# Kernel tuning notes

Measured on AMD Instinct MI355X. Metric: run time of the kernel, lower is better.

## Reference

```python
import jax, jax.numpy as jnp
import numpy as np

DIM = 512
H = 8
D = 64
EPS = 1e-5


def _ln(x, g, b):
    m = jnp.mean(x, axis=-1, keepdims=True)
    v = jnp.var(x, axis=-1, keepdims=True)
    return (x - m) * jax.lax.rsqrt(v + EPS) * g + b


def _attn(x, ctx, wq, wk, wv, wo, bo):
    B, S, _ = x.shape
    T = ctx.shape[1]
    q = (x @ wq).reshape(B, S, H, D)
    k = (ctx @ wk).reshape(B, T, H, D)
    v = (ctx @ wv).reshape(B, T, H, D)
    scale = D ** -0.5
    score = jnp.einsum('bqhd,bkhd->bhqk', q, k) * scale  # [B,H,S,T]
    w = jax.nn.softmax(score, axis=-1)
    o = jnp.einsum('bhqk,bkhd->bqhd', w, v).reshape(B, S, H * D)
    return o @ wo + bo


def _geglu(x, w, b):
    h = x @ w + b
    y, gate = h[..., :4 * DIM], h[..., 4 * DIM:]
    tanh_res = jnp.tanh(gate * 0.7978845608 * (1.0 + 0.044715 * gate * gate))
    return y * 0.5 * gate * (1.0 + tanh_res)


def setup_inputs() -> dict:
    key = jax.random.key(0)
    ks = jax.random.split(key, 16)
    s = 0.02
    inp = {
        'x': jax.random.normal(ks[0], (2, 4096, DIM), jnp.float32),
        'context': jax.random.normal(ks[1], (2, 77, DIM), jnp.float32),
        'ln1_g': jnp.ones((DIM,), jnp.float32),
        'ln1_b': jnp.zeros((DIM,), jnp.float32),
        'wq1': jax.random.normal(ks[2], (DIM, H * D), jnp.float32) * s,
        'wk1': jax.random.normal(ks[3], (DIM, H * D), jnp.float32) * s,
        'wv1': jax.random.normal(ks[4], (DIM, H * D), jnp.float32) * s,
        'wo1': jax.random.normal(ks[5], (H * D, H * D), jnp.float32) * s,
        'bo1': jnp.zeros((H * D,), jnp.float32),
        'ln2_g': jnp.ones((DIM,), jnp.float32),
        'ln2_b': jnp.zeros((DIM,), jnp.float32),
        'wq2': jax.random.normal(ks[6], (DIM, H * D), jnp.float32) * s,
        'wk2': jax.random.normal(ks[7], (DIM, H * D), jnp.float32) * s,
        'wv2': jax.random.normal(ks[8], (DIM, H * D), jnp.float32) * s,
        'wo2': jax.random.normal(ks[9], (H * D, H * D), jnp.float32) * s,
        'bo2': jnp.zeros((H * D,), jnp.float32),
        'ln3_g': jnp.ones((DIM,), jnp.float32),
        'ln3_b': jnp.zeros((DIM,), jnp.float32),
        'geglu_w': jax.random.normal(ks[10], (DIM, 8 * DIM), jnp.float32) * s,
        'geglu_b': jnp.zeros((8 * DIM,), jnp.float32),
        'out_w': jax.random.normal(ks[11], (4 * DIM, DIM), jnp.float32) * s,
        'out_b': jnp.zeros((DIM,), jnp.float32),
    }
    return inp


def reference(x, context, ln1_g, ln1_b, wq1, wk1, wv1, wo1, bo1,
              ln2_g, ln2_b, wq2, wk2, wv2, wo2, bo2,
              ln3_g, ln3_b, geglu_w, geglu_b, out_w, out_b):
    h = _attn(_ln(x, ln1_g, ln1_b), _ln(x, ln1_g, ln1_b), wq1, wk1, wv1, wo1, bo1) + x
    h = _attn(_ln(h, ln2_g, ln2_b), context, wq2, wk2, wv2, wo2, bo2) + h
    ff = _geglu(_ln(h, ln3_g, ln3_b), geglu_w, geglu_b)
    return ff @ out_w + out_b + h
```

## Files before the change

### kernel.cpp

```cpp
#include <hip/hip_runtime.h>
#include <hip/hip_bf16.h>
#include <math.h>

#define DIM 512
#define NHEAD 8
#define HD 64
#define BATCH 2
#define SEQ 4096
#define CTXLEN 77
#define NTOK (BATCH*SEQ)
#define NCTX (BATCH*CTXLEN)

typedef __hip_bfloat16 bf16;
typedef __attribute__((ext_vector_type(8))) short bf8_t;
typedef __attribute__((ext_vector_type(4))) float f4_t;

__device__ __forceinline__ float b2f(bf16 v){ return __bfloat162float(v); }
__device__ __forceinline__ bf16  f2b(float v){ return __float2bfloat16(v); }
__device__ __forceinline__ unsigned int packbf2(float a, float b){
    unsigned int au = __float_as_uint(a) + 0x8000u;
    unsigned int bu = __float_as_uint(b) + 0x8000u;
    return __builtin_amdgcn_perm(bu, au, 0x07060302u);
}
__device__ __forceinline__ void  stf(float* p, float v){ *p = v; }
__device__ __forceinline__ void  stf(bf16* p, float v){ *p = f2b(v); }

__device__ __forceinline__ void glds16(const bf16* g, unsigned short* l){
    __builtin_amdgcn_global_load_lds(
        (__attribute__((address_space(1))) void*)g,
        (__attribute__((address_space(3))) void*)l,
        16, 0, 0);
}

__global__ __launch_bounds__(256)
void ln_kernel(const float* __restrict__ x, const float* __restrict__ g,
               const float* __restrict__ b, bf16* __restrict__ out, int nrows)
{
    int row  = blockIdx.x * 4 + (threadIdx.x >> 6);
    int lane = threadIdx.x & 63;
    if (row >= nrows) return;
    const float* xr = x + (size_t)row * DIM;
    float v[8];
    float s = 0.f, sq = 0.f;
    #pragma unroll
    for (int j = 0; j < 8; ++j) {
        float f = xr[lane + 64*j];
        v[j] = f; s += f; sq += f*f;
    }
    #pragma unroll
    for (int off = 32; off; off >>= 1) {
        s  += __shfl_xor(s,  off);
        sq += __shfl_xor(sq, off);
    }
    float mean = s * (1.f/DIM);
    float var  = sq * (1.f/DIM) - mean*mean;
    float rstd = rsqrtf(var + 1e-5f);
    bf16* orow = out + (size_t)row * DIM;
    #pragma unroll
    for (int j = 0; j < 8; ++j) {
        int c = lane + 64*j;
        orow[c] = f2b((v[j]-mean)*rstd*g[c] + b[c]);
    }
}

__global__ __launch_bounds__(256)
void transpose_bf16_kernel(const float* __restrict__ W, bf16* __restrict__ Wt, int K, int N)
{
    __shared__ float tile[32][33];
    int n0 = blockIdx.x * 32, k0 = blockIdx.y * 32;
    int tx = threadIdx.x & 31, ty = threadIdx.x >> 5;
    #pragma unroll
    for (int p = 0; p < 4; ++p)
        tile[ty + p*8][tx] = W[(size_t)(k0 + ty + p*8)*N + n0 + tx];
    __syncthreads();
    #pragma unroll
    for (int p = 0; p < 4; ++p)
        Wt[(size_t)(n0 + ty + p*8)*K + k0 + tx] = f2b(tile[tx][ty + p*8]);
}

struct TPtrs { const float* src[8]; bf16* dst[8]; };
__global__ __launch_bounds__(256)
void transpose8_kernel(TPtrs p)
{
    __shared__ float tile[32][33];
    const float* W = p.src[blockIdx.z];
    bf16* Wt = p.dst[blockIdx.z];
    int n0 = blockIdx.x * 32, k0 = blockIdx.y * 32;
    int tx = threadIdx.x & 31, ty = threadIdx.x >> 5;
    #pragma unroll
    for (int q = 0; q < 4; ++q)
        tile[ty + q*8][tx] = W[(size_t)(k0 + ty + q*8)*512 + n0 + tx];
    __syncthreads();
    #pragma unroll
    for (int q = 0; q < 4; ++q)
        Wt[(size_t)(n0 + ty + q*8)*512 + k0 + tx] = f2b(tile[tx][ty + q*8]);
}

__global__ __launch_bounds__(256)
void cast_bf16_kernel(const float* __restrict__ in, bf16* __restrict__ out, int n)
{
    int i = blockIdx.x*256 + threadIdx.x;
    if (i < n) out[i] = f2b(in[i]);
}

__global__ __launch_bounds__(256)
void v_transpose_kernel(const bf16* __restrict__ V, bf16* __restrict__ Vt, int T, int pitch)
{
    __shared__ __align__(16) unsigned short tile[64*64];
    const int tid = threadIdx.x;
    const int b = blockIdx.z, h = blockIdx.y;
    const int t0 = blockIdx.x * 64;
    #pragma unroll
    for (int it = 0; it < 2; ++it) {
        int e = tid + it*256;
        int t = e >> 3, c = e & 7;
        int gk = t0 + t;
        bf8_t v = {0,0,0,0,0,0,0,0};
        if (gk < T) v = *(const bf8_t*)(V + ((size_t)(b*T + gk))*DIM + h*HD + c*8);
        *(bf8_t*)&tile[t*64 + c*8] = v;
    }
    __syncthreads();
    #pragma unroll
    for (int it = 0; it < 2; ++it) {
        int e = tid + it*256;
        int d = e & 63, oc = e >> 6;
        unsigned short tmp[8];
        #pragma unroll
        for (int j = 0; j < 8; ++j) tmp[j] = tile[(oc*8 + j)*64 + d];
        *(bf8_t*)(Vt + ((size_t)((b*8 + h)*64 + d))*pitch + t0 + oc*8) = *(bf8_t*)tmp;
    }
}

struct OutPtrs { void* p[3]; };
template<int RESID, typename OUTT, bool GUARD>
__global__ __launch_bounds__(256)
void gemm_mfma_kernel(const bf16* __restrict__ A, const bf16* __restrict__ Wt,
                      const float* __restrict__ bias, const float* __restrict__ resid,
                      OutPtrs outs, int M, int K)
{
    __shared__ __align__(16) unsigned short As[2][128*64];
    __shared__ __align__(16) unsigned short Bs[2][64*64];
    const int tid  = threadIdx.x;
    const int wave = tid >> 6, lane = tid & 63;
    const int l16  = lane & 15, quad = lane >> 4;
    const int wm = (wave >> 1) * 64, wn = (wave & 1) * 32;
    const int m0 = blockIdx.y * 128, n0 = blockIdx.x * 64;
    OUTT* outp = (OUTT*)outs.p[n0 >> 9];
    const int lc0 = n0 & 511;
    const int lr = lane >> 3;
    const int lc = (lane & 7) ^ lr;

    f4_t acc[4][2];
    #pragma unroll
    for (int i = 0; i < 4; ++i) { acc[i][0] = f4_t{0,0,0,0}; acc[i][1] = f4_t{0,0,0,0}; }

    auto stage = [&](int k0, int bf) {
        #pragma unroll
        for (int i = 0; i < 4; ++i) {
            int r = (wave*4 + i)*8 + lr;
            int gr = m0 + r;
            if (GUARD) gr = (gr < M) ? gr : (M-1);
            glds16(A + (size_t)gr*K + k0 + lc*8, &As[bf][(wave*4 + i)*512]);
        }
        #pragma unroll
        for (int j = 0; j < 2; ++j) {
            int r = (wave*2 + j)*8 + lr;
            glds16(Wt + (size_t)(n0 + r)*K + k0 + lc*8, &Bs[bf][(wave*2 + j)*512]);
        }
    };

    stage(0, 0);
    __syncthreads();

    for (int k0 = 0; k0 < K; k0 += 64) {
        const int bf = (k0 >> 6) & 1;
        if (k0 + 64 < K) stage(k0 + 64, bf ^ 1);
        #pragma unroll
        for (int kc = 0; kc < 2; ++kc) {
            const int cg = kc*4 + quad;
            bf8_t af[4], bfr[2];
            #pragma unroll
            for (int mt = 0; mt < 4; ++mt) {
                int r = wm + mt*16 + l16;
                af[mt] = *(const bf8_t*)&As[bf][r*64 + ((cg ^ (r&7))*8)];
            }
            #pragma unroll
            for (int nt = 0; nt < 2; ++nt) {
                int r = wn + nt*16 + l16;
                bfr[nt] = *(const bf8_t*)&Bs[bf][r*64 + ((cg ^ (r&7))*8)];
            }
            #pragma unroll
            for (int mt = 0; mt < 4; ++mt)
                #pragma unroll
                for (int nt = 0; nt < 2; ++nt)
                    acc[mt][nt] = __builtin_amdgcn_mfma_f32_16x16x32_bf16(af[mt], bfr[nt], acc[mt][nt], 0, 0, 0);
        }
        __syncthreads();
    }

    #pragma unroll
    for (int mt = 0; mt < 4; ++mt) {
        #pragma unroll
        for (int r_ = 0; r_ < 4; ++r_) {
            int row = m0 + wm + mt*16 + quad*4 + r_;
            if (GUARD && row >= M) continue;
            size_t rb = (size_t)row * 512;
            #pragma unroll
            for (int nt = 0; nt < 2; ++nt) {
                int col = lc0 + wn + nt*16 + l16;
                float v = acc[mt][nt][r_];
                if (bias) v += bias[col];
                if (RESID) v += resid[rb + col];
                stf(&outp[rb + col], v);
            }
        }
    }
}

__global__ __launch_bounds__(256)
void geglu_mfma_kernel(const bf16* __restrict__ A, const bf16* __restrict__ WtG,
                       const float* __restrict__ bias, bf16* __restrict__ outp)
{
    __shared__ __align__(16) unsigned short As[128*64];
    __shared__ __align__(16) unsigned short Bys[64*64];
    __shared__ __align__(16) unsigned short Bgs[64*64];
    const int tid  = threadIdx.x;
    const int wave = tid >> 6, lane = tid & 63;
    const int l16  = lane & 15, quad = lane >> 4;
    const int m0 = blockIdx.y * 128, n0 = blockIdx.x * 64;
    const int lr = lane >> 3;
    const int lc = (lane & 7) ^ lr;

    f4_t accy[2][4], accg[2][4];
    #pragma unroll
    for (int i = 0; i < 2; ++i)
        #pragma unroll
        for (int j = 0; j < 4; ++j) { accy[i][j] = f4_t{0,0,0,0}; accg[i][j] = f4_t{0,0,0,0}; }

    for (int k0 = 0; k0 < DIM; k0 += 64) {
        #pragma unroll
        for (int i = 0; i < 4; ++i) {
            int r = (wave*4 + i)*8 + lr;
            glds16(A + (size_t)(m0 + r)*DIM + k0 + lc*8, &As[(wave*4 + i)*512]);
        }
        #pragma unroll
        for (int j = 0; j < 2; ++j) {
            int r = (wave*2 + j)*8 + lr;
            glds16(WtG + (size_t)(n0 + r)*DIM + k0 + lc*8, &Bys[(wave*2 + j)*512]);
            glds16(WtG + (size_t)(2048 + n0 + r)*DIM + k0 + lc*8, &Bgs[(wave*2 + j)*512]);
        }
        __syncthreads();
        #pragma unroll
        for (int kc = 0; kc < 2; ++kc) {
            const int cg = kc*4 + quad;
            bf8_t af[2];
            #pragma unroll
            for (int mt = 0; mt < 2; ++mt) {
                int r = wave*32 + mt*16 + l16;
                af[mt] = *(const bf8_t*)&As[r*64 + ((cg ^ (r&7))*8)];
            }
            #pragma unroll
            for (int nt = 0; nt < 4; ++nt) {
                int r = nt*16 + l16;
                bf8_t by = *(const bf8_t*)&Bys[r*64 + ((cg ^ (r&7))*8)];
                bf8_t bg = *(const bf8_t*)&Bgs[r*64 + ((cg ^ (r&7))*8)];
                #pragma unroll
                for (int mt = 0; mt < 2; ++mt) {
                    accy[mt][nt] = __builtin_amdgcn_mfma_f32_16x16x32_bf16(af[mt], by, accy[mt][nt], 0, 0, 0);
                    accg[mt][nt] = __builtin_amdgcn_mfma_f32_16x16x32_bf16(af[mt], bg, accg[mt][nt], 0, 0, 0);
                }
            }
        }
        __syncthreads();
    }

    #pragma unroll
    for (int mt = 0; mt < 2; ++mt) {
        #pragma unroll
        for (int r_ = 0; r_ < 4; ++r_) {
            int row = m0 + wave*32 + mt*16 + quad*4 + r_;
            size_t rb = (size_t)row * 2048;
            #pragma unroll
            for (int nt = 0; nt < 4; ++nt) {
                int col = n0 + nt*16 + l16;
                float y = accy[mt][nt][r_] + bias[col];
                float g = accg[mt][nt][r_] + bias[2048 + col];
                float t = tanhf(0.7978845608f*g*(1.f + 0.044715f*g*g));
                outp[rb + col] = f2b(y * 0.5f * g * (1.f + t));
            }
        }
    }
}

__global__ __launch_bounds__(512)
void attn_mfma_kernel(const bf16* __restrict__ Qm, const bf16* __restrict__ Km,
                      const bf16* __restrict__ VtG, bf16* __restrict__ Om,
                      int T, int vpitch)
{
    __shared__ __align__(16) unsigned short Ks[2][64*64];
    __shared__ __align__(16) unsigned short Vts[2][64*64];

    const int tid  = threadIdx.x;
    const int wave = tid >> 6, lane = tid & 63;
    const int l16  = lane & 15, quad = lane >> 4;
    const int b = blockIdx.z, h = blockIdx.y;
    const int qblk = blockIdx.x * 128;
    const int lr = lane >> 3;
    const int lc = (lane & 7) ^ lr;
    const int srow = wave*8 + lr;

    bf8_t ones;
    #pragma unroll
    for (int j = 0; j < 8; ++j) ((unsigned short*)&ones)[j] = 0x3F80;

    bf8_t qf[2];
    {
        const bf16* qp = Qm + ((size_t)(b*SEQ + qblk + wave*16 + l16))*DIM + h*HD + quad*8;
        #pragma unroll
        for (int kc = 0; kc < 2; ++kc) {
            bf8_t v = *(const bf8_t*)(qp + kc*32);
            unsigned short* u = (unsigned short*)&v;
            unsigned int* w = (unsigned int*)&v;
            #pragma unroll
            for (int j = 0; j < 4; ++j) {
                float f0 = b2f(*(bf16*)&u[2*j])   * 0.1803368801f;
                float f1 = b2f(*(bf16*)&u[2*j+1]) * 0.1803368801f;
                w[j] = packbf2(f0, f1);
            }
            qf[kc] = v;
        }
    }

    f4_t o[4];
    #pragma unroll
    for (int dt = 0; dt < 4; ++dt) o[dt] = f4_t{0,0,0,0};
    f4_t lacc = {0,0,0,0};

    const bf16* Kbase = Km + (size_t)b*T*DIM + h*HD;
    const bf16* Vbase = VtG + ((size_t)((b*8 + h)*64 + srow))*vpitch;

    {
        int gk = srow; if (gk > T-1) gk = T-1;
        glds16(Kbase + (size_t)gk*DIM + lc*8, &Ks[0][wave*512]);
        glds16(Vbase + lc*8,                  &Vts[0][wave*512]);
    }
    __syncthreads();

    const int ntiles = (T + 63) >> 6;
    for (int t0 = 0; t0 < ntiles; ++t0) {
        const int kb = t0 << 6;
        const int cur = t0 & 1;
        if (t0 + 1 < ntiles) {
            int gk = kb + 64 + srow; if (gk > T-1) gk = T-1;
            glds16(Kbase + (size_t)gk*DIM + lc*8,  &Ks[cur^1][wave*512]);
            glds16(Vbase + kb + 64 + lc*8,         &Vts[cur^1][wave*512]);
        }

        bf8_t kf[4][2], vf[4][2];
        #pragma unroll
        for (int t = 0; t < 4; ++t) {
            int r = t*16 + l16;
            #pragma unroll
            for (int kc = 0; kc < 2; ++kc) {
                int cg = kc*4 + quad;
                kf[t][kc] = *(const bf8_t*)&Ks[cur][r*64 + ((cg ^ (r&7))*8)];
                vf[t][kc] = *(const bf8_t*)&Vts[cur][r*64 + ((cg ^ (r&7))*8)];
            }
        }
        const bool tail = (kb + 64 > T);

        f4_t sc4[4];
        #pragma unroll
        for (int km = 0; km < 4; ++km) {
            f4_t c = {0,0,0,0};
            c = __builtin_amdgcn_mfma_f32_16x16x32_bf16(kf[km][0], qf[0], c, 0, 0, 0);
            c = __builtin_amdgcn_mfma_f32_16x16x32_bf16(kf[km][1], qf[1], c, 0, 0, 0);
            sc4[km] = c;
        }
        if (tail) {
            #pragma unroll
            for (int km = 0; km < 4; ++km)
                #pragma unroll
                for (int r = 0; r < 4; ++r)
                    if (kb + km*16 + quad*4 + r >= T) sc4[km][r] = -1e30f;
        }
        unsigned int pk[4][2];
        #pragma unroll
        for (int km = 0; km < 4; ++km) {
            pk[km][0] = packbf2(exp2f(sc4[km][0]), exp2f(sc4[km][1]));
            pk[km][1] = packbf2(exp2f(sc4[km][2]), exp2f(sc4[km][3]));
        }
        #pragma unroll
        for (int kc = 0; kc < 2; ++kc) {
            auto s0 = __builtin_amdgcn_permlane32_swap(pk[2*kc][0], pk[2*kc+1][0], false, false);
            auto w02 = __builtin_amdgcn_permlane16_swap(s0[0], s0[1], false, false);
            auto s1 = __builtin_amdgcn_permlane32_swap(pk[2*kc][1], pk[2*kc+1][1], false, false);
            auto w13 = __builtin_amdgcn_permlane16_swap(s1[0], s1[1], false, false);
            union { unsigned int u[4]; bf8_t v; } pfu;
            pfu.u[0] = w02[0]; pfu.u[1] = w13[0]; pfu.u[2] = w02[1]; pfu.u[3] = w13[1];
            bf8_t pf = pfu.v;
            lacc = __builtin_amdgcn_mfma_f32_16x16x32_bf16(ones, pf, lacc, 0, 0, 0);
            #pragma unroll
            for (int dt = 0; dt < 4; ++dt)
                o[dt] = __builtin_amdgcn_mfma_f32_16x16x32_bf16(vf[dt][kc], pf, o[dt], 0, 0, 0);
        }
        __syncthreads();
    }

    {
        float inv = 1.f / lacc[0];
        int tok = qblk + wave*16 + l16;
        size_t base = ((size_t)(b*SEQ + tok))*DIM + h*HD;
        #pragma unroll
        for (int dt = 0; dt < 4; ++dt) {
            uint2 w;
            w.x = packbf2(o[dt][0]*inv, o[dt][1]*inv);
            w.y = packbf2(o[dt][2]*inv, o[dt][3]*inv);
            *(uint2*)(Om + base + dt*16 + quad*4) = w;
        }
    }
}

extern "C" void kernel_launch(void* const* d_in, const int* in_sizes, int n_in,
                              void* d_out, int out_size, void* d_ws, size_t ws_size,
                              hipStream_t stream)
{
    (void)in_sizes; (void)n_in; (void)out_size; (void)ws_size;
    const float* x    = (const float*)d_in[0];
    const float* ctx  = (const float*)d_in[1];
    const float* ln1g = (const float*)d_in[2];
    const float* ln1b = (const float*)d_in[3];
    const float* wq1  = (const float*)d_in[4];
    const float* wk1  = (const float*)d_in[5];
    const float* wv1  = (const float*)d_in[6];
    const float* wo1  = (const float*)d_in[7];
    const float* bo1  = (const float*)d_in[8];
    const float* ln2g = (const float*)d_in[9];
    const float* ln2b = (const float*)d_in[10];
    const float* wq2  = (const float*)d_in[11];
    const float* wk2  = (const float*)d_in[12];
    const float* wv2  = (const float*)d_in[13];
    const float* wo2  = (const float*)d_in[14];
    const float* bo2  = (const float*)d_in[15];
    const float* ln3g = (const float*)d_in[16];
    const float* ln3b = (const float*)d_in[17];
    const float* gw   = (const float*)d_in[18];
    const float* gb   = (const float*)d_in[19];
    const float* ow   = (const float*)d_in[20];
    const float* ob   = (const float*)d_in[21];
    float* out = (float*)d_out;

    char* ws = (char*)d_ws;
    bf16* An  = (bf16*)(ws);
    bf16* VtG = (bf16*)(ws);
    bf16* Qb  = (bf16*)(ws + ((size_t)8<<20));
    bf16* Kb  = (bf16*)(ws + ((size_t)16<<20));
    bf16* Vb  = (bf16*)(ws + ((size_t)24<<20));
    bf16* Ob  = (bf16*)(ws + ((size_t)32<<20));
    bf16* FF  = Qb;
    float* Hf = out;
    bf16* WT  = (bf16*)(ws + ((size_t)40<<20));
    bf16* wq1T = WT + 0*262144, *wk1T = WT + 1*262144, *wv1T = WT + 2*262144, *wo1T = WT + 3*262144;
    bf16* wq2T = WT + 4*262144, *wk2T = WT + 5*262144, *wv2T = WT + 6*262144, *wo2T = WT + 7*262144;
    bf16* gwT  = (bf16*)(ws + ((size_t)44<<20));
    bf16* owT  = (bf16*)(ws + ((size_t)48<<20));
    bf16* ctxb = (bf16*)(ws + ((size_t)50<<20));
    bf16* VtG2 = (bf16*)(ws + ((size_t)50<<20) + ((size_t)512<<10));

    dim3 blk(256);
    dim3 blkA(512);

    TPtrs tp;
    tp.src[0]=wq1; tp.src[1]=wk1; tp.src[2]=wv1; tp.src[3]=wo1;
    tp.src[4]=wq2; tp.src[5]=wk2; tp.src[6]=wv2; tp.src[7]=wo2;
    tp.dst[0]=wq1T; tp.dst[1]=wk1T; tp.dst[2]=wv1T; tp.dst[3]=wo1T;
    tp.dst[4]=wq2T; tp.dst[5]=wk2T; tp.dst[6]=wv2T; tp.dst[7]=wo2T;
    transpose8_kernel<<<dim3(16,16,8), blk, 0, stream>>>(tp);
    transpose_bf16_kernel<<<dim3(128,16), blk, 0, stream>>>(gw, gwT, DIM, 4096);
    transpose_bf16_kernel<<<dim3(16,64), blk, 0, stream>>>(ow, owT, 2048, DIM);
    cast_bf16_kernel<<<dim3((NCTX*DIM+255)/256), blk, 0, stream>>>(ctx, ctxb, NCTX*DIM);

    dim3 gLN(NTOK/4);
    dim3 gQKV(24, 64);
    dim3 gG(8, 64);
    dim3 gKVx(16, 2);
    dim3 gGEGLU(32, 64);
    dim3 gATT(SEQ/128, NHEAD, BATCH);
    OutPtrs oQKV{{Qb, Kb, Vb}};
    OutPtrs oKVx{{Kb, Vb, nullptr}};
    OutPtrs oQ{{Qb, nullptr, nullptr}};
    OutPtrs oH{{Hf, nullptr, nullptr}};
    OutPtrs oOut{{out, nullptr, nullptr}};

    ln_kernel<<<gLN, blk, 0, stream>>>(x, ln1g, ln1b, An, NTOK);
    gemm_mfma_kernel<0,bf16,false><<<gQKV, blk, 0, stream>>>(An, wq1T, nullptr, nullptr, oQKV, NTOK, DIM);
    v_transpose_kernel<<<dim3(SEQ/64, NHEAD, BATCH), blk, 0, stream>>>(Vb, VtG, SEQ, SEQ);
    attn_mfma_kernel<<<gATT, blkA, 0, stream>>>(Qb, Kb, VtG, Ob, SEQ, SEQ);
    gemm_mfma_kernel<1,float,false><<<gG, blk, 0, stream>>>(Ob, wo1T, bo1, x, oH, NTOK, DIM);

    ln_kernel<<<gLN, blk, 0, stream>>>(Hf, ln2g, ln2b, An, NTOK);
    gemm_mfma_kernel<0,bf16,false><<<gG, blk, 0, stream>>>(An, wq2T, nullptr, nullptr, oQ, NTOK, DIM);
    gemm_mfma_kernel<0,bf16,true><<<gKVx, blk, 0, stream>>>(ctxb, wk2T, nullptr, nullptr, oKVx, NCTX, DIM);
    v_transpose_kernel<<<dim3(2, NHEAD, BATCH), blk, 0, stream>>>(Vb, VtG2, CTXLEN, 128);
    attn_mfma_kernel<<<gATT, blkA, 0, stream>>>(Qb, Kb, VtG2, Ob, CTXLEN, 128);
    gemm_mfma_kernel<1,float,false><<<gG, blk, 0, stream>>>(Ob, wo2T, bo2, Hf, oH, NTOK, DIM);

    ln_kernel<<<gLN, blk, 0, stream>>>(Hf, ln3g, ln3b, An, NTOK);
    geglu_mfma_kernel<<<gGEGLU, blk, 0, stream>>>(An, gwT, gb, FF);
    gemm_mfma_kernel<1,float,false><<<gG, blk, 0, stream>>>(FF, owT, ob, Hf, oOut, NTOK, 2048);
}
```

Measured before the change: 472.2 us.

## Split self-attention over two key halves with a combine pass, restructure K/V staging

The self-attention kernel now splits the key range into two halves across extra blocks, writes unnormalized fp32 partial outputs and row sums, and a new combine kernel sums and normalizes them. The aim is more blocks and more parallelism for the long-sequence attention. K/V staging switches from double-buffered async global-to-LDS loads to register prefetch into a single LDS buffer. The P-matrix transpose moves from permlane swaps to an LDS round-trip. The price is extra fp32 partial-output traffic, one more launch, and an extra sync plus LDS writes per tile.

```diff
diff --git a/kernel.cpp b/kernel.cpp
--- a/kernel.cpp
+++ b/kernel.cpp
@@ -292,22 +292,26 @@
     }
 }
 
-__global__ __launch_bounds__(512)
+template<bool SPLITW>
+__global__ __launch_bounds__(512, 8)
 void attn_mfma_kernel(const bf16* __restrict__ Qm, const bf16* __restrict__ Km,
                       const bf16* __restrict__ VtG, bf16* __restrict__ Om,
+                      float* __restrict__ OP, float* __restrict__ LP,
                       int T, int vpitch)
 {
-    __shared__ __align__(16) unsigned short Ks[2][64*64];
-    __shared__ __align__(16) unsigned short Vts[2][64*64];
+    __shared__ __align__(16) unsigned short Ks[64*64];
+    __shared__ __align__(16) unsigned short Vts[64*64];
+    __shared__ __align__(16) unsigned short Ps[8][16*64];
 
     const int tid  = threadIdx.x;
     const int wave = tid >> 6, lane = tid & 63;
     const int l16  = lane & 15, quad = lane >> 4;
-    const int b = blockIdx.z, h = blockIdx.y;
+    int b, s, TT, t_lo;
+    if (SPLITW) { s = blockIdx.z >> 1; b = blockIdx.z & 1; TT = T >> 1; t_lo = s * TT; }
+    else        { s = 0; b = blockIdx.z; TT = T; t_lo = 0; }
+    const int h = blockIdx.y;
     const int qblk = blockIdx.x * 128;
-    const int lr = lane >> 3;
-    const int lc = (lane & 7) ^ lr;
-    const int srow = wave*8 + lr;
+    const int sr = tid >> 3, sc_ = tid & 7;
 
     bf8_t ones;
     #pragma unroll
@@ -336,24 +340,25 @@
     for (int dt = 0; dt < 4; ++dt) o[dt] = f4_t{0,0,0,0};
     f4_t lacc = {0,0,0,0};
 
-    const bf16* Kbase = Km + (size_t)b*T*DIM + h*HD;
-    const bf16* Vbase = VtG + ((size_t)((b*8 + h)*64 + srow))*vpitch;
-
-    {
-        int gk = srow; if (gk > T-1) gk = T-1;
-        glds16(Kbase + (size_t)gk*DIM + lc*8, &Ks[0][wave*512]);
-        glds16(Vbase + lc*8,                  &Vts[0][wave*512]);
-    }
-    __syncthreads();
-
-    const int ntiles = (T + 63) >> 6;
+    const bf16* Kbase = Km + ((size_t)b*T + t_lo)*DIM + h*HD;
+    const bf16* Vbase = VtG + ((size_t)((b*8 + h)*64 + sr))*vpitch + t_lo;
+
+    bf8_t kq, vq;
+    kq = bf8_t{0,0,0,0,0,0,0,0};
+    if (sr < TT) kq = *(const bf8_t*)(Kbase + (size_t)sr*DIM + sc_*8);
+    vq = *(const bf8_t*)(Vbase + sc_*8);
+
+    const int ntiles = (TT + 63) >> 6;
     for (int t0 = 0; t0 < ntiles; ++t0) {
         const int kb = t0 << 6;
-        const int cur = t0 & 1;
+        *(bf8_t*)&Ks[sr*64 + ((sc_ ^ (sr&7))*8)]  = kq;
+        *(bf8_t*)&Vts[sr*64 + ((sc_ ^ (sr&7))*8)] = vq;
+        __syncthreads();
         if (t0 + 1 < ntiles) {
-            int gk = kb + 64 + srow; if (gk > T-1) gk = T-1;
-            glds16(Kbase + (size_t)gk*DIM + lc*8,  &Ks[cur^1][wave*512]);
-            glds16(Vbase + kb + 64 + lc*8,         &Vts[cur^1][wave*512]);
+            int gk = kb + 64 + sr;
+            kq = bf8_t{0,0,0,0,0,0,0,0};
+            if (gk < TT) kq = *(const bf8_t*)(Kbase + (size_t)gk*DIM + sc_*8);
+            vq = *(const bf8_t*)(Vbase + kb + 64 + sc_*8);
         }
 
         bf8_t kf[4][2], vf[4][2];
@@ -363,11 +368,11 @@
             #pragma unroll
             for (int kc = 0; kc < 2; ++kc) {
                 int cg = kc*4 + quad;
-                kf[t][kc] = *(const bf8_t*)&Ks[cur][r*64 + ((cg ^ (r&7))*8)];
-                vf[t][kc] = *(const bf8_t*)&Vts[cur][r*64 + ((cg ^ (r&7))*8)];
-            }
-        }
-        const bool tail = (kb + 64 > T);
+                kf[t][kc] = *(const bf8_t*)&Ks[r*64 + ((cg ^ (r&7))*8)];
+                vf[t][kc] = *(const bf8_t*)&Vts[r*64 + ((cg ^ (r&7))*8)];
+            }
+        }
+        const bool tail = (kb + 64 > TT);
 
         f4_t sc4[4];
         #pragma unroll
@@ -382,23 +387,21 @@
             for (int km = 0; km < 4; ++km)
                 #pragma unroll
                 for (int r = 0; r < 4; ++r)
-                    if (kb + km*16 + quad*4 + r >= T) sc4[km][r] = -1e30f;
-        }
-        unsigned int pk[4][2];
+                    if (kb + km*16 + quad*4 + r >= TT) sc4[km][r] = -1e30f;
+        }
         #pragma unroll
         for (int km = 0; km < 4; ++km) {
-            pk[km][0] = packbf2(exp2f(sc4[km][0]), exp2f(sc4[km][1]));
-            pk[km][1] = packbf2(exp2f(sc4[km][2]), exp2f(sc4[km][3]));
+            uint2 w;
+            w.x = packbf2(exp2f(sc4[km][0]), exp2f(sc4[km][1]));
+            w.y = packbf2(exp2f(sc4[km][2]), exp2f(sc4[km][3]));
+            int chunk = 2*km + (quad >> 1);
+            int a = l16*64 + ((chunk ^ (l16 & 7))*8) + (quad & 1)*4;
+            *(uint2*)&Ps[wave][a] = w;
         }
         #pragma unroll
         for (int kc = 0; kc < 2; ++kc) {
-            auto s0 = __builtin_amdgcn_permlane32_swap(pk[2*kc][0], pk[2*kc+1][0], false, false);
-            auto w02 = __builtin_amdgcn_permlane16_swap(s0[0], s0[1], false, false);
-            auto s1 = __builtin_amdgcn_permlane32_swap(pk[2*kc][1], pk[2*kc+1][1], false, false);
-            auto w13 = __builtin_amdgcn_permlane16_swap(s1[0], s1[1], false, false);
-            union { unsigned int u[4]; bf8_t v; } pfu;
-            pfu.u[0] = w02[0]; pfu.u[1] = w13[0]; pfu.u[2] = w02[1]; pfu.u[3] = w13[1];
-            bf8_t pf = pfu.v;
+            int cg = kc*4 + quad;
+            bf8_t pf = *(const bf8_t*)&Ps[wave][l16*64 + ((cg ^ (l16 & 7))*8)];
             lacc = __builtin_amdgcn_mfma_f32_16x16x32_bf16(ones, pf, lacc, 0, 0, 0);
             #pragma unroll
             for (int dt = 0; dt < 4; ++dt)
@@ -407,9 +410,16 @@
         __syncthreads();
     }
 
-    {
+    const int tok = qblk + wave*16 + l16;
+    if (SPLITW) {
+        size_t obase = ((size_t)((s*BATCH + b)*SEQ) + tok)*DIM + h*HD;
+        #pragma unroll
+        for (int dt = 0; dt < 4; ++dt)
+            *(f4_t*)(OP + obase + dt*16 + quad*4) = o[dt];
+        if (quad == 0)
+            LP[((size_t)((s*BATCH + b)*SEQ) + tok)*NHEAD + h] = lacc[0];
+    } else {
         float inv = 1.f / lacc[0];
-        int tok = qblk + wave*16 + l16;
         size_t base = ((size_t)(b*SEQ + tok))*DIM + h*HD;
         #pragma unroll
         for (int dt = 0; dt < 4; ++dt) {
@@ -419,6 +429,26 @@
             *(uint2*)(Om + base + dt*16 + quad*4) = w;
         }
     }
+}
+
+__global__ __launch_bounds__(256)
+void attn_combine_kernel(const float* __restrict__ OP, const float* __restrict__ LP,
+                         bf16* __restrict__ Om)
+{
+    const size_t NP = (size_t)BATCH*SEQ*DIM;
+    int i = blockIdx.x*256 + threadIdx.x;
+    size_t e = (size_t)i * 4;
+    int bt = (int)(e >> 9);
+    int d  = (int)(e & 511);
+    int hh = d >> 6;
+    f4_t a0 = *(const f4_t*)(OP + (size_t)bt*DIM + d);
+    f4_t a1 = *(const f4_t*)(OP + NP + (size_t)bt*DIM + d);
+    float l = LP[(size_t)bt*NHEAD + hh] + LP[(size_t)BATCH*SEQ*NHEAD + (size_t)bt*NHEAD + hh];
+    float inv = 1.f / l;
+    uint2 w;
+    w.x = packbf2((a0[0]+a1[0])*inv, (a0[1]+a1[1])*inv);
+    w.y = packbf2((a0[2]+a1[2])*inv, (a0[3]+a1[3])*inv);
+    *(uint2*)(Om + e) = w;
 }
 
 extern "C" void kernel_launch(void* const* d_in, const int* in_sizes, int n_in,
@@ -466,6 +496,8 @@
     bf16* owT  = (bf16*)(ws + ((size_t)48<<20));
     bf16* ctxb = (bf16*)(ws + ((size_t)50<<20));
     bf16* VtG2 = (bf16*)(ws + ((size_t)50<<20) + ((size_t)512<<10));
+    float* OP  = (float*)(ws + ((size_t)52<<20));
+    float* LP  = (float*)(ws + ((size_t)86<<20));
 
     dim3 blk(256);
     dim3 blkA(512);
@@ -486,6 +518,8 @@
     dim3 gKVx(16, 2);
     dim3 gGEGLU(32, 64);
     dim3 gATT(SEQ/128, NHEAD, BATCH);
+    dim3 gATTs(SEQ/128, NHEAD, BATCH*2);
+    dim3 gCMB(NTOK*DIM/4/256);
     OutPtrs oQKV{{Qb, Kb, Vb}};
     OutPtrs oKVx{{Kb, Vb, nullptr}};
     OutPtrs oQ{{Qb, nullptr, nullptr}};
@@ -495,14 +529,15 @@
     ln_kernel<<<gLN, blk, 0, stream>>>(x, ln1g, ln1b, An, NTOK);
     gemm_mfma_kernel<0,bf16,false><<<gQKV, blk, 0, stream>>>(An, wq1T, nullptr, nullptr, oQKV, NTOK, DIM);
     v_transpose_kernel<<<dim3(SEQ/64, NHEAD, BATCH), blk, 0, stream>>>(Vb, VtG, SEQ, SEQ);
-    attn_mfma_kernel<<<gATT, blkA, 0, stream>>>(Qb, Kb, VtG, Ob, SEQ, SEQ);
+    attn_mfma_kernel<true><<<gATTs, blkA, 0, stream>>>(Qb, Kb, VtG, Ob, OP, LP, SEQ, SEQ);
+    attn_combine_kernel<<<gCMB, blk, 0, stream>>>(OP, LP, Ob);
     gemm_mfma_kernel<1,float,false><<<gG, blk, 0, stream>>>(Ob, wo1T, bo1, x, oH, NTOK, DIM);
 
     ln_kernel<<<gLN, blk, 0, stream>>>(Hf, ln2g, ln2b, An, NTOK);
     gemm_mfma_kernel<0,bf16,false><<<gG, blk, 0, stream>>>(An, wq2T, nullptr, nullptr, oQ, NTOK, DIM);
     gemm_mfma_kernel<0,bf16,true><<<gKVx, blk, 0, stream>>>(ctxb, wk2T, nullptr, nullptr, oKVx, NCTX, DIM);
     v_transpose_kernel<<<dim3(2, NHEAD, BATCH), blk, 0, stream>>>(Vb, VtG2, CTXLEN, 128);
-    attn_mfma_kernel<<<gATT, blkA, 0, stream>>>(Qb, Kb, VtG2, Ob, CTXLEN, 128);
+    attn_mfma_kernel<false><<<gATT, blkA, 0, stream>>>(Qb, Kb, VtG2, Ob, nullptr, nullptr, CTXLEN, 128);
     gemm_mfma_kernel<1,float,false><<<gG, blk, 0, stream>>>(Ob, wo2T, bo2, Hf, oH, NTOK, DIM);
 
     ln_kernel<<<gLN, blk, 0, stream>>>(Hf, ln3g, ln3b, An, NTOK);
```

After: 1.173 ms. +148.4%, slower.
